# Optimization experiments

Hardware: AMD Instinct MI355X
Metric: run time of the kernel (lower is better)

Reference implementation:

```python
import jax, jax.numpy as jnp
import numpy as np

B, N, D, P = 8, 64, 256, 256   # batch, nodes, input_features, proj_size_filler (== proj_size_role)
E = N * (N - 1)                # complete directed graph


def _layer_norm(x, g, b, eps=1e-5):
    mu = jnp.mean(x, axis=-1, keepdims=True)
    v = jnp.mean((x - mu) ** 2, axis=-1, keepdims=True)
    return (x - mu) * jax.lax.rsqrt(v + eps) * g + b


def _lin_init(k, fin, fout):
    k1, k2 = jax.random.split(k)
    lim = 1.0 / np.sqrt(fin)
    W = jax.random.uniform(k1, (fin, fout), minval=-lim, maxval=lim, dtype=jnp.float32)
    b = jax.random.uniform(k2, (fout,), minval=-lim, maxval=lim, dtype=jnp.float32)
    return W, b


def setup_inputs() -> dict:
    key = jax.random.key(0)
    ks = jax.random.split(key, 10)
    # complete directed graph, src-major order: node i -> all j != i
    src = np.repeat(np.arange(N), N - 1)
    mesh = np.tile(np.arange(N), (N, 1))
    dst = mesh[~np.eye(N, dtype=bool)].reshape(N, N - 1).ravel()
    edge_index = np.broadcast_to(np.stack([src, dst])[None], (B, 2, E)).copy()
    W_f0, b_f0 = _lin_init(ks[0], 3 * D, D)
    W_f1, b_f1 = _lin_init(ks[1], D, D)
    W_f2, b_f2 = _lin_init(ks[2], D, P)
    W_i0, b_i0 = _lin_init(ks[3], 2 * D + P, D)
    W_i1, b_i1 = _lin_init(ks[4], D, D)
    W_i2, b_i2 = _lin_init(ks[5], D, D)
    return {
        "node_features": jax.random.normal(ks[6], (B, N, D), dtype=jnp.float32),
        "edge_features": jax.random.normal(ks[7], (B, E, D), dtype=jnp.float32),
        "target_node": jax.random.normal(ks[8], (B, D), dtype=jnp.float32),
        "edge_index": jnp.asarray(edge_index, dtype=jnp.int32),
        "W_f0": W_f0, "b_f0": b_f0, "W_f1": W_f1, "b_f1": b_f1, "W_f2": W_f2, "b_f2": b_f2,
        "ln_gamma": jnp.ones((P,), jnp.float32), "ln_beta": jnp.zeros((P,), jnp.float32),
        "W_i0": W_i0, "b_i0": b_i0, "W_i1": W_i1, "b_i1": b_i1, "W_i2": W_i2, "b_i2": b_i2,
    }


def reference(node_features, edge_features, target_node, edge_index,
              W_f0, b_f0, W_f1, b_f1, W_f2, b_f2, ln_gamma, ln_beta,
              W_i0, b_i0, W_i1, b_i1, W_i2, b_i2):
    src = edge_index[:, 0, :]                                   # [B,E]
    dst = edge_index[:, 1, :]                                   # [B,E]
    nf_src = jnp.take_along_axis(node_features, src[..., None], axis=1)  # [B,E,D]
    nf_dst = jnp.take_along_axis(node_features, dst[..., None], axis=1)  # [B,E,D]
    # --- initialization: edge-wise MLP (original calls x.relu() without assignment ->
    # no activation; dropout is eval-mode identity) ---
    h = jnp.concatenate([nf_src, edge_features, nf_dst], axis=-1)        # [B,E,3D]
    h = h @ W_f0 + b_f0
    h = h @ W_f1 + b_f1
    filler = h @ W_f2 + b_f2                                             # [B,E,P]
    # scatter-add of per-edge outer products into node memory; edges are src-major
    # (node i owns edges i*(N-1):(i+1)*(N-1)) so the segment-sum is a block reshape.
    mem = jnp.einsum('bnep,bned->bnpd',
                     filler.reshape(B, N, N - 1, P),
                     nf_dst.reshape(B, N, N - 1, D))                     # [B,N,P,D]
    # --- propagation: complete graph => every pair adjacent => BFS yields only
    # trivial length-1 paths, which collect_long_dependancy ignores (identity). ---
    # --- inference ---
    retrieved = jnp.einsum('bnpd,bd->bnp', mem, target_node)             # [B,N,P]
    retrieved = _layer_norm(retrieved, ln_gamma, ln_beta)
    tgt = jnp.broadcast_to(target_node[:, None, :], (B, N, D))
    z = jnp.concatenate([node_features, retrieved, tgt], axis=-1)        # [B,N,2D+P]
    z = z @ W_i0 + b_i0
    z = z @ W_i1 + b_i1
    z = z @ W_i2 + b_i2                                                  # [B,N,D]
    return z
```

## Files before the change

kernel.cpp:

```cpp
#include <hip/hip_runtime.h>

#define BB 8
#define NN 64
#define DD 256
#define PP 256
#define NE 63
#define EE 4032

__global__ __launch_bounds__(64) void k_dot(const float* __restrict__ nf,
                                            const float* __restrict__ tgt,
                                            float* __restrict__ dotv) {
    int row = blockIdx.x;
    int b = row >> 6;
    int lane = threadIdx.x;
    const float4* x4 = (const float4*)(nf + (size_t)row * DD);
    const float4* t4 = (const float4*)(tgt + (size_t)b * DD);
    float4 a = x4[lane];
    float4 c = t4[lane];
    float acc = a.x * c.x + a.y * c.y + a.z * c.z + a.w * c.w;
#pragma unroll
    for (int off = 32; off; off >>= 1) acc += __shfl_down(acc, off, 64);
    if (lane == 0) dotv[row] = acc;
}

__global__ __launch_bounds__(512) void k_edge(const float* __restrict__ nf,
                                              const float* __restrict__ ef,
                                              const int* __restrict__ eidx,
                                              const float* __restrict__ dotv,
                                              float* __restrict__ conc,
                                              float* __restrict__ Svec) {
    __shared__ float s_sh[NE];
    __shared__ int src_sh[NE];
    __shared__ int dst_sh[NE];
    __shared__ float Pat[2][256], Pus[2][256], Pud[2][256];
    int bn = blockIdx.x;
    int b = bn >> 6, n = bn & 63;
    int tid = threadIdx.x;
    int t = tid & 255;
    int h = tid >> 8;
    if (tid < NE) {
        const int* srcp = eidx + (size_t)b * 2 * EE + n * NE;
        int si = srcp[tid];
        int di = srcp[EE + tid];
        src_sh[tid] = si;
        dst_sh[tid] = di;
        s_sh[tid] = dotv[(b << 6) + di];
    }
    __syncthreads();
    const float* efp = ef + ((size_t)b * EE + (size_t)n * NE) * DD + t;
    const float* nfb = nf + ((size_t)(b << 6)) * DD + t;
    float at = 0.f, aus = 0.f, aud = 0.f;
    int e0 = h ? 32 : 0;
    int e1 = h ? 63 : 32;
#pragma unroll 8
    for (int e = e0; e < e1; ++e) {
        float sv = s_sh[e];
        at  += sv * efp[(size_t)e * DD];
        aus += sv * nfb[(size_t)src_sh[e] * DD];
        aud += sv * nfb[(size_t)dst_sh[e] * DD];
    }
    Pat[h][t] = at; Pus[h][t] = aus; Pud[h][t] = aud;
    __syncthreads();
    if (h == 0) {
        float* o = conc + (size_t)bn * 768;
        o[t]       = Pus[0][t] + Pus[1][t];
        o[256 + t] = Pat[0][t] + Pat[1][t];
        o[512 + t] = Pud[0][t] + Pud[1][t];
        if (t == 0) {
            float S = 0.f;
            for (int e = 0; e < NE; ++e) S += s_sh[e];
            Svec[bn] = S;
        }
    }
}

__global__ __launch_bounds__(1024) void k_mlp(const float* __restrict__ conc,
                                              const float* __restrict__ Svec,
                                              const float* __restrict__ nf,
                                              const float* __restrict__ tgt,
                                              const float* __restrict__ Wf0, const float* __restrict__ bf0,
                                              const float* __restrict__ Wf1, const float* __restrict__ bf1,
                                              const float* __restrict__ Wf2, const float* __restrict__ bf2,
                                              const float* __restrict__ gam, const float* __restrict__ bet,
                                              const float* __restrict__ Wi0, const float* __restrict__ bi0,
                                              const float* __restrict__ Wi1, const float* __restrict__ bi1,
                                              const float* __restrict__ Wi2, const float* __restrict__ bi2,
                                              float* __restrict__ outp) {
    __shared__ float A[4 * 768];
    __shared__ float Z[4 * 768];
    __shared__ float P[4][4 * 256];
    __shared__ float H[4 * 256];
    __shared__ float red1[16], red2[16];
    int r0 = blockIdx.x * 4;
    int tid = threadIdx.x;
    int j = tid & 255;
    int h = tid >> 8;

    for (int i = tid; i < 4 * 768; i += 1024) A[i] = conc[(size_t)r0 * 768 + i];
    {
        int row = r0 + h;
        Z[h * 768 + j]       = nf[(size_t)row * DD + j];
        Z[h * 768 + 512 + j] = tgt[(size_t)(row >> 6) * DD + j];
    }
    float Sv[4];
#pragma unroll
    for (int r = 0; r < 4; ++r) Sv[r] = Svec[r0 + r];
    __syncthreads();

    auto layer = [&](const float* X, int xs, int K, const float* __restrict__ W,
                     const float* __restrict__ bias, bool scaleS,
                     float* OUT, bool store) -> float {
        int kpart = K >> 2;
        const float* Wp = W + (size_t)h * kpart * 256 + j;
        const float* Xp = X + h * kpart;
        float a0 = 0.f, a1 = 0.f, a2 = 0.f, a3 = 0.f;
#pragma unroll 16
        for (int k = 0; k < kpart; ++k) {
            float w = Wp[(size_t)k * 256];
            a0 += Xp[k] * w;
            a1 += Xp[xs + k] * w;
            a2 += Xp[2 * xs + k] * w;
            a3 += Xp[3 * xs + k] * w;
        }
        float* Pp = P[h];
        Pp[j] = a0; Pp[256 + j] = a1; Pp[512 + j] = a2; Pp[768 + j] = a3;
        __syncthreads();
        int rj = h * 256 + j;
        float v = P[0][rj] + P[1][rj] + P[2][rj] + P[3][rj];
        v += (scaleS ? Sv[h] : 1.f) * bias[j];
        if (store) {
            OUT[rj] = v;
            __syncthreads();
        }
        return v;
    };

    layer(A, 768, 768, Wf0, bf0, true, H, true);
    layer(H, 256, 256, Wf1, bf1, true, H, true);
    float v = layer(H, 256, 256, Wf2, bf2, true, nullptr, false);

    {
        float s1 = v, s2 = v * v;
#pragma unroll
        for (int off = 32; off; off >>= 1) {
            s1 += __shfl_down(s1, off, 64);
            s2 += __shfl_down(s2, off, 64);
        }
        int wv = (tid >> 6) & 3;
        if ((tid & 63) == 0) { red1[h * 4 + wv] = s1; red2[h * 4 + wv] = s2; }
        __syncthreads();
        float sum = red1[h * 4] + red1[h * 4 + 1] + red1[h * 4 + 2] + red1[h * 4 + 3];
        float sq  = red2[h * 4] + red2[h * 4 + 1] + red2[h * 4 + 2] + red2[h * 4 + 3];
        float mu  = sum * (1.f / 256.f);
        float var = sq * (1.f / 256.f) - mu * mu;
        float inv = rsqrtf(var + 1e-5f);
        Z[h * 768 + 256 + j] = (v - mu) * inv * gam[j] + bet[j];
        __syncthreads();
    }

    layer(Z, 768, 768, Wi0, bi0, false, H, true);
    layer(H, 256, 256, Wi1, bi1, false, H, true);
    float o = layer(H, 256, 256, Wi2, bi2, false, nullptr, false);
    outp[(size_t)(r0 + h) * 256 + j] = o;
}

extern "C" void kernel_launch(void* const* d_in, const int* in_sizes, int n_in,
                              void* d_out, int out_size, void* d_ws, size_t ws_size,
                              hipStream_t stream) {
    const float* nf  = (const float*)d_in[0];
    const float* ef  = (const float*)d_in[1];
    const float* tgt = (const float*)d_in[2];
    const int*   ei  = (const int*)d_in[3];
    const float* Wf0 = (const float*)d_in[4];
    const float* bf0 = (const float*)d_in[5];
    const float* Wf1 = (const float*)d_in[6];
    const float* bf1 = (const float*)d_in[7];
    const float* Wf2 = (const float*)d_in[8];
    const float* bf2 = (const float*)d_in[9];
    const float* gam = (const float*)d_in[10];
    const float* bet = (const float*)d_in[11];
    const float* Wi0 = (const float*)d_in[12];
    const float* bi0 = (const float*)d_in[13];
    const float* Wi1 = (const float*)d_in[14];
    const float* bi1 = (const float*)d_in[15];
    const float* Wi2 = (const float*)d_in[16];
    const float* bi2 = (const float*)d_in[17];
    float* out = (float*)d_out;

    float* dotv = (float*)d_ws;
    float* Svec = dotv + 512;
    float* conc = Svec + 512;

    k_dot<<<BB * NN, 64, 0, stream>>>(nf, tgt, dotv);
    k_edge<<<BB * NN, 512, 0, stream>>>(nf, ef, ei, dotv, conc, Svec);
    k_mlp<<<(BB * NN) / 4, 1024, 0, stream>>>(conc, Svec, nf, tgt,
                                              Wf0, bf0, Wf1, bf1, Wf2, bf2,
                                              gam, bet, Wi0, bi0, Wi1, bi1, Wi2, bi2,
                                              out);
}
```

Measured before the change: 151.8 us.

## Fuse dot kernel into edge kernel, vectorize edge and MLP loops

```diff
diff --git a/kernel.cpp b/kernel.cpp
--- a/kernel.cpp
+++ b/kernel.cpp
@@ -7,70 +7,77 @@
 #define NE 63
 #define EE 4032
 
-__global__ __launch_bounds__(64) void k_dot(const float* __restrict__ nf,
-                                            const float* __restrict__ tgt,
-                                            float* __restrict__ dotv) {
-    int row = blockIdx.x;
-    int b = row >> 6;
-    int lane = threadIdx.x;
-    const float4* x4 = (const float4*)(nf + (size_t)row * DD);
-    const float4* t4 = (const float4*)(tgt + (size_t)b * DD);
-    float4 a = x4[lane];
-    float4 c = t4[lane];
-    float acc = a.x * c.x + a.y * c.y + a.z * c.z + a.w * c.w;
-#pragma unroll
-    for (int off = 32; off; off >>= 1) acc += __shfl_down(acc, off, 64);
-    if (lane == 0) dotv[row] = acc;
-}
-
 __global__ __launch_bounds__(512) void k_edge(const float* __restrict__ nf,
                                               const float* __restrict__ ef,
                                               const int* __restrict__ eidx,
-                                              const float* __restrict__ dotv,
                                               float* __restrict__ conc,
-                                              float* __restrict__ Svec) {
+                                              float* __restrict__ Svec,
+                                              const float* __restrict__ tgt) {
     __shared__ float s_sh[NE];
     __shared__ int src_sh[NE];
     __shared__ int dst_sh[NE];
-    __shared__ float Pat[2][256], Pus[2][256], Pud[2][256];
+    __shared__ float Psh[8 * 768];
     int bn = blockIdx.x;
     int b = bn >> 6, n = bn & 63;
     int tid = threadIdx.x;
-    int t = tid & 255;
-    int h = tid >> 8;
+    int lane = tid & 63;
+    int h = tid >> 6;
+
     if (tid < NE) {
         const int* srcp = eidx + (size_t)b * 2 * EE + n * NE;
-        int si = srcp[tid];
-        int di = srcp[EE + tid];
-        src_sh[tid] = si;
-        dst_sh[tid] = di;
-        s_sh[tid] = dotv[(b << 6) + di];
-    }
-    __syncthreads();
-    const float* efp = ef + ((size_t)b * EE + (size_t)n * NE) * DD + t;
-    const float* nfb = nf + ((size_t)(b << 6)) * DD + t;
-    float at = 0.f, aus = 0.f, aud = 0.f;
-    int e0 = h ? 32 : 0;
-    int e1 = h ? 63 : 32;
-#pragma unroll 8
-    for (int e = e0; e < e1; ++e) {
+        src_sh[tid] = srcp[tid];
+        dst_sh[tid] = srcp[EE + tid];
+    }
+    __syncthreads();
+
+    const float4* nf4  = (const float4*)nf;
+    const float4* tgt4 = (const float4*)(tgt + (size_t)b * DD);
+    float4 c4 = tgt4[lane];
+
+    int eA0 = h * 8, eA1 = min(NE, h * 8 + 8);
+    for (int e = eA0; e < eA1; ++e) {
+        int d = dst_sh[e];
+        float4 a4 = nf4[(size_t)((b << 6) + d) * 64 + lane];
+        float p = a4.x * c4.x + a4.y * c4.y + a4.z * c4.z + a4.w * c4.w;
+#pragma unroll
+        for (int off = 32; off; off >>= 1) p += __shfl_down(p, off, 64);
+        if (lane == 0) s_sh[e] = p;
+    }
+    __syncthreads();
+
+    if (tid < 64) {
+        float v = (tid < NE) ? s_sh[tid] : 0.f;
+#pragma unroll
+        for (int off = 32; off; off >>= 1) v += __shfl_down(v, off, 64);
+        if (tid == 0) Svec[bn] = v;
+    }
+
+    const float4* ef4 = (const float4*)ef;
+    size_t efbase = ((size_t)b * EE + (size_t)n * NE) * 64 + lane;
+    size_t nfbase = (size_t)(b << 6) * 64 + lane;
+    float4 at = {0,0,0,0}, aus = {0,0,0,0}, aud = {0,0,0,0};
+#pragma unroll 4
+    for (int e = eA0; e < eA1; ++e) {
         float sv = s_sh[e];
-        at  += sv * efp[(size_t)e * DD];
-        aus += sv * nfb[(size_t)src_sh[e] * DD];
-        aud += sv * nfb[(size_t)dst_sh[e] * DD];
-    }
-    Pat[h][t] = at; Pus[h][t] = aus; Pud[h][t] = aud;
-    __syncthreads();
-    if (h == 0) {
-        float* o = conc + (size_t)bn * 768;
-        o[t]       = Pus[0][t] + Pus[1][t];
-        o[256 + t] = Pat[0][t] + Pat[1][t];
-        o[512 + t] = Pud[0][t] + Pud[1][t];
-        if (t == 0) {
-            float S = 0.f;
-            for (int e = 0; e < NE; ++e) S += s_sh[e];
-            Svec[bn] = S;
-        }
+        float4 fe = ef4[efbase + (size_t)e * 64];
+        float4 fs = nf4[nfbase + (size_t)src_sh[e] * 64];
+        float4 fd = nf4[nfbase + (size_t)dst_sh[e] * 64];
+        at.x += sv * fe.x; at.y += sv * fe.y; at.z += sv * fe.z; at.w += sv * fe.w;
+        aus.x += sv * fs.x; aus.y += sv * fs.y; aus.z += sv * fs.z; aus.w += sv * fs.w;
+        aud.x += sv * fd.x; aud.y += sv * fd.y; aud.z += sv * fd.z; aud.w += sv * fd.w;
+    }
+    float4* Pf4 = (float4*)Psh;
+    Pf4[(size_t)(h * 3 + 0) * 64 + lane] = aus;
+    Pf4[(size_t)(h * 3 + 1) * 64 + lane] = at;
+    Pf4[(size_t)(h * 3 + 2) * 64 + lane] = aud;
+    __syncthreads();
+
+    float* o = conc + (size_t)bn * 768;
+    for (int i = tid; i < 768; i += 512) {
+        float s = 0.f;
+#pragma unroll
+        for (int hh = 0; hh < 8; ++hh) s += Psh[hh * 768 + i];
+        o[i] = s;
     }
 }
 
@@ -86,58 +93,67 @@
                                               const float* __restrict__ Wi1, const float* __restrict__ bi1,
                                               const float* __restrict__ Wi2, const float* __restrict__ bi2,
                                               float* __restrict__ outp) {
-    __shared__ float A[4 * 768];
-    __shared__ float Z[4 * 768];
-    __shared__ float P[4][4 * 256];
-    __shared__ float H[4 * 256];
+    __shared__ float At[768 * 4];
+    __shared__ float Zt[768 * 4];
+    __shared__ float P[16 * 4 * 256];
+    __shared__ float Ht[256 * 4];
     __shared__ float red1[16], red2[16];
     int r0 = blockIdx.x * 4;
     int tid = threadIdx.x;
-    int j = tid & 255;
-    int h = tid >> 8;
-
-    for (int i = tid; i < 4 * 768; i += 1024) A[i] = conc[(size_t)r0 * 768 + i];
+    int jg = tid & 63;
+    int h = tid >> 6;
+    int col = tid & 255;
+    int r2 = tid >> 8;
+
     {
-        int row = r0 + h;
-        Z[h * 768 + j]       = nf[(size_t)row * DD + j];
-        Z[h * 768 + 512 + j] = tgt[(size_t)(row >> 6) * DD + j];
-    }
-    float Sv[4];
-#pragma unroll
-    for (int r = 0; r < 4; ++r) Sv[r] = Svec[r0 + r];
-    __syncthreads();
-
-    auto layer = [&](const float* X, int xs, int K, const float* __restrict__ W,
+        const float* cp = conc + (size_t)(r0 + r2) * 768;
+#pragma unroll
+        for (int q = 0; q < 3; ++q) {
+            int k = col + q * 256;
+            At[k * 4 + r2] = cp[k];
+        }
+        Zt[col * 4 + r2]         = nf[(size_t)(r0 + r2) * DD + col];
+        Zt[(512 + col) * 4 + r2] = tgt[(size_t)((r0 + r2) >> 6) * DD + col];
+    }
+    float Sv = Svec[r0 + r2];
+    __syncthreads();
+
+    auto layer = [&](const float* Xt, int K, const float* __restrict__ W,
                      const float* __restrict__ bias, bool scaleS,
-                     float* OUT, bool store) -> float {
-        int kpart = K >> 2;
-        const float* Wp = W + (size_t)h * kpart * 256 + j;
-        const float* Xp = X + h * kpart;
-        float a0 = 0.f, a1 = 0.f, a2 = 0.f, a3 = 0.f;
-#pragma unroll 16
+                     float* OUTt, bool store) -> float {
+        int kpart = K >> 4;
+        const float4* Wp = (const float4*)(W + (size_t)(h * kpart) * 256) + jg;
+        const float4* Xp = (const float4*)Xt + h * kpart;
+        float4 a0 = {0,0,0,0}, a1 = {0,0,0,0}, a2 = {0,0,0,0}, a3 = {0,0,0,0};
+#pragma unroll 8
         for (int k = 0; k < kpart; ++k) {
-            float w = Wp[(size_t)k * 256];
-            a0 += Xp[k] * w;
-            a1 += Xp[xs + k] * w;
-            a2 += Xp[2 * xs + k] * w;
-            a3 += Xp[3 * xs + k] * w;
-        }
-        float* Pp = P[h];
-        Pp[j] = a0; Pp[256 + j] = a1; Pp[512 + j] = a2; Pp[768 + j] = a3;
-        __syncthreads();
-        int rj = h * 256 + j;
-        float v = P[0][rj] + P[1][rj] + P[2][rj] + P[3][rj];
-        v += (scaleS ? Sv[h] : 1.f) * bias[j];
+            float4 w = Wp[(size_t)k * 64];
+            float4 x = Xp[k];
+            a0.x += x.x * w.x; a0.y += x.x * w.y; a0.z += x.x * w.z; a0.w += x.x * w.w;
+            a1.x += x.y * w.x; a1.y += x.y * w.y; a1.z += x.y * w.z; a1.w += x.y * w.w;
+            a2.x += x.z * w.x; a2.y += x.z * w.y; a2.z += x.z * w.z; a2.w += x.z * w.w;
+            a3.x += x.w * w.x; a3.y += x.w * w.y; a3.z += x.w * w.z; a3.w += x.w * w.w;
+        }
+        float4* Pf4 = (float4*)P;
+        Pf4[(size_t)(h * 4 + 0) * 64 + jg] = a0;
+        Pf4[(size_t)(h * 4 + 1) * 64 + jg] = a1;
+        Pf4[(size_t)(h * 4 + 2) * 64 + jg] = a2;
+        Pf4[(size_t)(h * 4 + 3) * 64 + jg] = a3;
+        __syncthreads();
+        float v = 0.f;
+#pragma unroll
+        for (int hh = 0; hh < 16; ++hh) v += P[(hh * 4 + r2) * 256 + col];
+        v += (scaleS ? Sv : 1.f) * bias[col];
         if (store) {
-            OUT[rj] = v;
-            __syncthreads();
-        }
+            OUTt[col * 4 + r2] = v;
+        }
+        __syncthreads();
         return v;
     };
 
-    layer(A, 768, 768, Wf0, bf0, true, H, true);
-    layer(H, 256, 256, Wf1, bf1, true, H, true);
-    float v = layer(H, 256, 256, Wf2, bf2, true, nullptr, false);
+    layer(At, 768, Wf0, bf0, true, Ht, true);
+    layer(Ht, 256, Wf1, bf1, true, Ht, true);
+    float v = layer(Ht, 256, Wf2, bf2, true, nullptr, false);
 
     {
         float s1 = v, s2 = v * v;
@@ -147,21 +163,21 @@
             s2 += __shfl_down(s2, off, 64);
         }
         int wv = (tid >> 6) & 3;
-        if ((tid & 63) == 0) { red1[h * 4 + wv] = s1; red2[h * 4 + wv] = s2; }
-        __syncthreads();
-        float sum = red1[h * 4] + red1[h * 4 + 1] + red1[h * 4 + 2] + red1[h * 4 + 3];
-        float sq  = red2[h * 4] + red2[h * 4 + 1] + red2[h * 4 + 2] + red2[h * 4 + 3];
+        if ((tid & 63) == 0) { red1[r2 * 4 + wv] = s1; red2[r2 * 4 + wv] = s2; }
+        __syncthreads();
+        float sum = red1[r2 * 4] + red1[r2 * 4 + 1] + red1[r2 * 4 + 2] + red1[r2 * 4 + 3];
+        float sq  = red2[r2 * 4] + red2[r2 * 4 + 1] + red2[r2 * 4 + 2] + red2[r2 * 4 + 3];
         float mu  = sum * (1.f / 256.f);
         float var = sq * (1.f / 256.f) - mu * mu;
         float inv = rsqrtf(var + 1e-5f);
-        Z[h * 768 + 256 + j] = (v - mu) * inv * gam[j] + bet[j];
-        __syncthreads();
-    }
-
-    layer(Z, 768, 768, Wi0, bi0, false, H, true);
-    layer(H, 256, 256, Wi1, bi1, false, H, true);
-    float o = layer(H, 256, 256, Wi2, bi2, false, nullptr, false);
-    outp[(size_t)(r0 + h) * 256 + j] = o;
+        Zt[(256 + col) * 4 + r2] = (v - mu) * inv * gam[col] + bet[col];
+        __syncthreads();
+    }
+
+    layer(Zt, 768, Wi0, bi0, false, Ht, true);
+    layer(Ht, 256, Wi1, bi1, false, Ht, true);
+    float o = layer(Ht, 256, Wi2, bi2, false, nullptr, false);
+    outp[(size_t)(r0 + r2) * 256 + col] = o;
 }
 
 extern "C" void kernel_launch(void* const* d_in, const int* in_sizes, int n_in,
@@ -187,12 +203,10 @@
     const float* bi2 = (const float*)d_in[17];
     float* out = (float*)d_out;
 
-    float* dotv = (float*)d_ws;
-    float* Svec = dotv + 512;
+    float* Svec = (float*)d_ws;
     float* conc = Svec + 512;
 
-    k_dot<<<BB * NN, 64, 0, stream>>>(nf, tgt, dotv);
-    k_edge<<<BB * NN, 512, 0, stream>>>(nf, ef, ei, dotv, conc, Svec);
+    k_edge<<<BB * NN, 512, 0, stream>>>(nf, ef, ei, conc, Svec, tgt);
     k_mlp<<<(BB * NN) / 4, 1024, 0, stream>>>(conc, Svec, nf, tgt,
                                               Wf0, bf0, Wf1, bf1, Wf2, bf2,
                                               gam, bet, Wi0, bi0, Wi1, bi1, Wi2, bi2,
```

Result: faster. 144.7 us (-4.6%).
